# Performance work log

Hardware: AMD Instinct MI355X
Metric: run time of the kernel (lower is better)

The kernel has to match this reference:

```python
import jax, jax.numpy as jnp
import numpy as np

N = 100000   # nodes
E = 1600000  # edges (avg degree 16)
D = 128      # input/output dim
H = 128      # hidden dim
EPS = 1e-5


def _lin_init(key, fan_in, shape):
    s = 1.0 / np.sqrt(fan_in)
    return jax.random.uniform(key, shape, jnp.float32, minval=-s, maxval=s)


def setup_inputs() -> dict:
    key = jax.random.key(0)
    ks = jax.random.split(key, 12)
    x = jax.random.normal(ks[0], (N, D), jnp.float32)
    edge_index = jax.random.randint(ks[1], (2, E), 0, N, dtype=jnp.int64)
    return {
        "x": x,
        "edge_index": edge_index,
        # SAGEConv 1: lin_l (on aggregated, with bias), lin_r (root, no bias)
        "Wl1": _lin_init(ks[2], D, (D, H)),
        "bl1": jnp.zeros((H,), jnp.float32),
        "Wr1": _lin_init(ks[3], D, (D, H)),
        # graph LayerNorm 1 affine
        "g1": jnp.ones((H,), jnp.float32),
        "b1": jnp.zeros((H,), jnp.float32),
        # SAGEConv 2
        "Wl2": _lin_init(ks[4], H, (H, D)),
        "bl2": jnp.zeros((D,), jnp.float32),
        "Wr2": _lin_init(ks[5], H, (H, D)),
        # graph LayerNorm 2 affine
        "g2": jnp.ones((D,), jnp.float32),
        "b2": jnp.zeros((D,), jnp.float32),
    }


def graph_layernorm(h, gamma, beta):
    # PyG norm.LayerNorm mode='graph': normalize over ALL nodes and channels.
    mu = h.mean()
    hc = h - mu
    var = (hc * hc).mean()
    return hc * jax.lax.rsqrt(var + EPS) * gamma + beta


def sage_mean(h, src, dst, Wl, bl, Wr):
    # mean-aggregate source features at destination nodes
    msg = h[src]                                            # [E, C] gather
    ssum = jax.ops.segment_sum(msg, dst, num_segments=N)    # [N, C]
    cnt = jax.ops.segment_sum(jnp.ones((src.shape[0], 1), h.dtype), dst,
                              num_segments=N)               # [N, 1]
    agg = ssum / jnp.maximum(cnt, 1.0)
    return agg @ Wl + bl + h @ Wr


def reference(x, edge_index, Wl1, bl1, Wr1, g1, b1, Wl2, bl2, Wr2, g2, b2):
    src, dst = edge_index[0], edge_index[1]
    res = x
    h = jax.nn.relu(graph_layernorm(sage_mean(x, src, dst, Wl1, bl1, Wr1), g1, b1))
    h = jax.nn.relu(graph_layernorm(sage_mean(h, src, dst, Wl2, bl2, Wr2), g2, b2))
    return h + res
```

## Files before the change

### kernel.cpp

```cpp
#include <hip/hip_runtime.h>

typedef float  f32x4 __attribute__((ext_vector_type(4)));
typedef float  f32x2 __attribute__((ext_vector_type(2)));
typedef short  s16x8 __attribute__((ext_vector_type(8)));

#define BSHIFT 7
#define BMASK  127
#define CHUNK  8192

__device__ __forceinline__ unsigned short f2bf(float f) {
  unsigned int u = __float_as_uint(f);
  unsigned int r = (u + 0x7FFFu + ((u >> 16) & 1u)) >> 16;
  return (unsigned short)r;
}

__device__ __forceinline__ uint2 pk8_fp8(const float* y) {
  int p0 = __builtin_amdgcn_cvt_pk_fp8_f32(y[0], y[1], 0, false);
  p0     = __builtin_amdgcn_cvt_pk_fp8_f32(y[2], y[3], p0, true);
  int p1 = __builtin_amdgcn_cvt_pk_fp8_f32(y[4], y[5], 0, false);
  p1     = __builtin_amdgcn_cvt_pk_fp8_f32(y[6], y[7], p1, true);
  return make_uint2((unsigned)p0, (unsigned)p1);
}


__global__ void __launch_bounds__(256) k_prep(
    const float* __restrict__ x, unsigned short* __restrict__ xh,
    unsigned int* __restrict__ xf8, size_t total8, int cvtBlocks,
    const float* __restrict__ W0, const float* __restrict__ W1,
    const float* __restrict__ W2, const float* __restrict__ W3,
    unsigned short* __restrict__ B0, unsigned short* __restrict__ B1,
    unsigned short* __restrict__ B2, unsigned short* __restrict__ B3,
    const int* __restrict__ ei, int E, int* __restrict__ bhist, int NB) {
  __shared__ int h[1024];
  int b = blockIdx.x;
  if (b < cvtBlocks) {
    size_t i = (size_t)b * 256 + threadIdx.x;
    if (i >= total8) return;
    float4 a = ((const float4*)x)[i * 2];
    float4 c = ((const float4*)x)[i * 2 + 1];
    uint4 o;
    o.x = (unsigned)f2bf(a.x) | ((unsigned)f2bf(a.y) << 16);
    o.y = (unsigned)f2bf(a.z) | ((unsigned)f2bf(a.w) << 16);
    o.z = (unsigned)f2bf(c.x) | ((unsigned)f2bf(c.y) << 16);
    o.w = (unsigned)f2bf(c.z) | ((unsigned)f2bf(c.w) << 16);
    ((uint4*)xh)[i] = o;
    float y[8] = {a.x, a.y, a.z, a.w, c.x, c.y, c.z, c.w};
    ((uint2*)xf8)[i] = pk8_fp8(y);
  } else if (b < cvtBlocks + 32) {
    int gt = (b - cvtBlocks) * 256 + threadIdx.x;
    int which = gt >> 11;
    const float* W = which == 0 ? W0 : which == 1 ? W1 : which == 2 ? W2 : W3;
    unsigned short* WB = which == 0 ? B0 : which == 1 ? B1 : which == 2 ? B2 : B3;
    int t = gt & 2047;
    int lane = t & 63, kt = (t >> 6) & 3, nt = t >> 8;
    int col = nt * 16 + (lane & 15);
    int k0  = kt * 32 + ((lane >> 4) << 3);
#pragma unroll
    for (int j = 0; j < 8; ++j)
      WB[(((nt * 4 + kt) * 64 + lane) << 3) + j] = f2bf(W[(size_t)(k0 + j) * 128 + col]);
  } else {
    int bb = b - cvtBlocks - 32;
    for (int i = threadIdx.x; i < 1024; i += 256) h[i] = 0;
    __syncthreads();
    int i0 = bb * 256 + threadIdx.x;
    int stride = 128 * 256;
    for (int e = i0; e < E; e += stride)
      atomicAdd(&h[ei[E + e] >> BSHIFT], 1);
    __syncthreads();
    for (int i = threadIdx.x; i < NB; i += 256)
      if (h[i]) atomicAdd(&bhist[i], h[i]);
  }
}


__global__ void k_bscan(const int* __restrict__ bhist, int* __restrict__ boff,
                        int* __restrict__ bcur, int NB, int E) {
  __shared__ int tot[256];
  int t = threadIdx.x;
  int v[4]; int s = 0;
#pragma unroll
  for (int j = 0; j < 4; ++j) {
    int idx = t * 4 + j;
    v[j] = (idx < NB) ? bhist[idx] : 0;
    s += v[j];
  }
  tot[t] = s; __syncthreads();
  for (int off = 1; off < 256; off <<= 1) {
    int x = (t >= off) ? tot[t - off] : 0;
    __syncthreads();
    tot[t] += x;
    __syncthreads();
  }
  int excl = (t > 0) ? tot[t - 1] : 0;
#pragma unroll
  for (int j = 0; j < 4; ++j) {
    int idx = t * 4 + j;
    if (idx < NB) { boff[idx] = excl; bcur[idx] = excl; }
    excl += v[j];
  }
  if (t == 0) boff[NB] = E;
}

__global__ void __launch_bounds__(512) k_part(
    const int* __restrict__ ei, int E, int* __restrict__ bcur,
    unsigned int* __restrict__ tmp, int NB) {
  __shared__ int lh[1024], lbase[1024], lcur[1024];
  int t = threadIdx.x;
  int c0 = blockIdx.x * CHUNK;
  int cend = min(c0 + CHUNK, E);
  for (int i = t; i < NB; i += 512) lh[i] = 0;
  __syncthreads();
  for (int e = c0 + t; e < cend; e += 512)
    atomicAdd(&lh[ei[E + e] >> BSHIFT], 1);
  __syncthreads();
  for (int i = t; i < NB; i += 512) {
    int c = lh[i];
    lbase[i] = c ? atomicAdd(&bcur[i], c) : 0;
    lcur[i] = 0;
  }
  __syncthreads();
  for (int e = c0 + t; e < cend; e += 512) {
    int src = ei[e], dst = ei[E + e];
    int b = dst >> BSHIFT;
    int pos = lbase[b] + atomicAdd(&lcur[b], 1);
    tmp[pos] = ((unsigned)(dst & BMASK) << 25) | (unsigned)src;
  }
}

__global__ void __launch_bounds__(256) k_csr(
    const unsigned int* __restrict__ tmp, const int* __restrict__ boff,
    int* __restrict__ rowptr, int* __restrict__ ssrc, int N, int NB, int E) {
  __shared__ int cnt[128], sc[128], curs[128];
  int b = blockIdx.x;
  int t = threadIdx.x;
  int beg = boff[b], end = boff[b + 1];
  int nbase = b << BSHIFT;
  int nn = min(128, N - nbase);
  if (t < 128) cnt[t] = 0;
  __syncthreads();
  for (int i = beg + t; i < end; i += 256)
    atomicAdd(&cnt[tmp[i] >> 25], 1);
  __syncthreads();
  if (t < 128) sc[t] = cnt[t];
  __syncthreads();
  for (int off = 1; off < 128; off <<= 1) {
    int x = 0;
    if (t < 128 && t >= off) x = sc[t - off];
    __syncthreads();
    if (t < 128) sc[t] += x;
    __syncthreads();
  }
  if (t < nn) {
    int excl = sc[t] - cnt[t];
    rowptr[nbase + t] = beg + excl;
    curs[t] = excl;
  }
  __syncthreads();
  for (int i = beg + t; i < end; i += 256) {
    unsigned int p = tmp[i];
    int pos = beg + atomicAdd(&curs[p >> 25], 1);
    ssrc[pos] = (int)((p & 0x1FFFFFFu) << 7);
  }
  if (b == NB - 1 && t == 0) rowptr[N] = E;
}


__global__ void __launch_bounds__(256, 8) k_fmm(
    const unsigned char* __restrict__ featf8, const unsigned short* __restrict__ featbf,
    const int* __restrict__ rowptr, const int* __restrict__ ssrc,
    const unsigned short* __restrict__ WlB, const unsigned short* __restrict__ WrB,
    const float* __restrict__ bias, unsigned short* __restrict__ out,
    double* __restrict__ red, int N) {
  __shared__ __align__(16) unsigned short aggLds[64 * 136];
  int t = threadIdx.x;
  int l = t & 63, w = t >> 6;
  const char* fp = (const char*)featf8;

  {
    int gg = l >> 3;
    int sub = l & 7;
    unsigned suboff = (unsigned)(sub * 16);
#pragma unroll
    for (int j = 0; j < 2; ++j) {
      int row = w * 16 + gg * 2 + j;
      int node = blockIdx.x * 64 + row;
      if (node < N) {
        int beg = rowptr[node], end = rowptr[node + 1];
        f32x2 a0 = {0.f, 0.f}, a1 = a0, a2 = a0, a3 = a0,
              a4 = a0, a5 = a0, a6 = a0, a7 = a0;
#define ACCQ(q) {                                                        \
          a0 += __builtin_amdgcn_cvt_pk_f32_fp8((q).x, false);           \
          a1 += __builtin_amdgcn_cvt_pk_f32_fp8((q).x, true);            \
          a2 += __builtin_amdgcn_cvt_pk_f32_fp8((q).y, false);           \
          a3 += __builtin_amdgcn_cvt_pk_f32_fp8((q).y, true);            \
          a4 += __builtin_amdgcn_cvt_pk_f32_fp8((q).z, false);           \
          a5 += __builtin_amdgcn_cvt_pk_f32_fp8((q).z, true);            \
          a6 += __builtin_amdgcn_cvt_pk_f32_fp8((q).w, false);           \
          a7 += __builtin_amdgcn_cvt_pk_f32_fp8((q).w, true);            \
        }
        int i = beg;
        for (; i + 4 <= end; i += 4) {
          unsigned o0 = (unsigned)ssrc[i]     + suboff;
          unsigned o1 = (unsigned)ssrc[i + 1] + suboff;
          unsigned o2 = (unsigned)ssrc[i + 2] + suboff;
          unsigned o3 = (unsigned)ssrc[i + 3] + suboff;
          uint4 q0 = *(const uint4*)(fp + o0);
          uint4 q1 = *(const uint4*)(fp + o1);
          uint4 q2 = *(const uint4*)(fp + o2);
          uint4 q3 = *(const uint4*)(fp + o3);
          ACCQ(q0); ACCQ(q1); ACCQ(q2); ACCQ(q3);
        }
        for (; i < end; ++i) {
          uint4 q = *(const uint4*)(fp + ((unsigned)ssrc[i] + suboff));
          ACCQ(q);
        }
#undef ACCQ
        float inv = __builtin_amdgcn_rcpf(fmaxf((float)(end - beg), 1.0f));
        uint4 oa, ob;
        oa.x = (unsigned)f2bf(a0.x * inv) | ((unsigned)f2bf(a0.y * inv) << 16);
        oa.y = (unsigned)f2bf(a1.x * inv) | ((unsigned)f2bf(a1.y * inv) << 16);
        oa.z = (unsigned)f2bf(a2.x * inv) | ((unsigned)f2bf(a2.y * inv) << 16);
        oa.w = (unsigned)f2bf(a3.x * inv) | ((unsigned)f2bf(a3.y * inv) << 16);
        ob.x = (unsigned)f2bf(a4.x * inv) | ((unsigned)f2bf(a4.y * inv) << 16);
        ob.y = (unsigned)f2bf(a5.x * inv) | ((unsigned)f2bf(a5.y * inv) << 16);
        ob.z = (unsigned)f2bf(a6.x * inv) | ((unsigned)f2bf(a6.y * inv) << 16);
        ob.w = (unsigned)f2bf(a7.x * inv) | ((unsigned)f2bf(a7.y * inv) << 16);
        *(uint4*)&aggLds[row * 136 + sub * 16] = oa;
        *(uint4*)&aggLds[row * 136 + sub * 16 + 8] = ob;
      } else {
        uint4 z = make_uint4(0, 0, 0, 0);
        *(uint4*)&aggLds[row * 136 + sub * 16] = z;
        *(uint4*)&aggLds[row * 136 + sub * 16 + 8] = z;
      }
    }
  }

  int r0 = blockIdx.x * 64 + w * 16;
  int c = l & 15;
  int rb = (l >> 4) << 2;
  int rowA = r0 + c;
  int rowAc = min(rowA, N - 1);
  const size_t goff = (size_t)rowAc * 128 + ((l >> 4) << 3);
  const unsigned short* aLds = &aggLds[(w * 16 + c) * 136 + ((l >> 4) << 3)];

  f32x4 acc[8];
#pragma unroll
  for (int nt = 0; nt < 8; ++nt) acc[nt] = (f32x4){0.f, 0.f, 0.f, 0.f};

#pragma unroll
  for (int kt = 0; kt < 4; ++kt) {
    s16x8 a = *(const s16x8*)(aLds + kt * 32);
#pragma unroll
    for (int nt = 0; nt < 8; ++nt) {
      s16x8 b;
      { uint4 q = *(const uint4*)(WlB + (((nt * 4 + kt) * 64 + l) << 3));
        b = *(const s16x8*)&q; }
      acc[nt] = __builtin_amdgcn_mfma_f32_16x16x32_bf16(a, b, acc[nt], 0, 0, 0);
    }
  }
#pragma unroll
  for (int kt = 0; kt < 4; ++kt) {
    s16x8 a;
    { uint4 q = *(const uint4*)(featbf + goff + kt * 32);
      a = *(const s16x8*)&q; }
#pragma unroll
    for (int nt = 0; nt < 8; ++nt) {
      s16x8 b;
      { uint4 q = *(const uint4*)(WrB + (((nt * 4 + kt) * 64 + l) << 3));
        b = *(const s16x8*)&q; }
      acc[nt] = __builtin_amdgcn_mfma_f32_16x16x32_bf16(a, b, acc[nt], 0, 0, 0);
    }
  }

  float s = 0.f, s2 = 0.f;
#pragma unroll
  for (int nt = 0; nt < 8; ++nt) {
    float bv = bias[nt * 16 + c];
#pragma unroll
    for (int i = 0; i < 4; ++i) {
      float v = acc[nt][i] + bv;
      if (r0 + rb + i < N) { s += v; s2 += v * v; }
      aggLds[(w * 16 + rb + i) * 136 + nt * 16 + c] = f2bf(v);
    }
  }

#pragma unroll
  for (int j = 0; j < 4; ++j) {
    int idx = j * 64 + l;
    int riw = idx >> 4;
    int chunk = idx & 15;
    int row = r0 + riw;
    if (row < N) {
      uint4 o = *(const uint4*)&aggLds[(w * 16 + riw) * 136 + chunk * 8];
      *(uint4*)(out + (size_t)row * 128 + chunk * 8) = o;
    }
  }

#pragma unroll
  for (int off = 1; off < 64; off <<= 1) {
    s  += __shfl_xor(s, off);
    s2 += __shfl_xor(s2, off);
  }
  if (l == 0) {
    int bucket = (blockIdx.x * 4 + w) & 255;
    atomicAdd(&red[2 * bucket],     (double)s);
    atomicAdd(&red[2 * bucket + 1], (double)s2);
  }
}


__global__ void __launch_bounds__(256) k_apply1(
    const unsigned short* __restrict__ h, unsigned short* __restrict__ o,
    unsigned int* __restrict__ of8,
    const double* __restrict__ red, double count,
    const float* __restrict__ gamma, const float* __restrict__ beta,
    size_t total8) {
  __shared__ double sh[256], sh2[256];
  __shared__ float sc[2];
  int t = threadIdx.x;
  sh[t] = red[2 * t]; sh2[t] = red[2 * t + 1];
  __syncthreads();
  for (int off = 128; off > 0; off >>= 1) {
    if (t < off) { sh[t] += sh[t + off]; sh2[t] += sh2[t + off]; }
    __syncthreads();
  }
  if (t == 0) {
    double mu = sh[0] / count;
    double var = sh2[0] / count - mu * mu;
    sc[0] = (float)mu;
    sc[1] = (float)(1.0 / sqrt(var + 1e-5));
  }
  __syncthreads();
  size_t i = (size_t)blockIdx.x * blockDim.x + t;
  if (i >= total8) return;
  float mu = sc[0], rs = sc[1];
  int c0 = (int)((i * 8) & 127);
  float4 g0 = *(const float4*)(gamma + c0);
  float4 g1 = *(const float4*)(gamma + c0 + 4);
  float4 b0 = *(const float4*)(beta + c0);
  float4 b1 = *(const float4*)(beta + c0 + 4);
  uint4 q = ((const uint4*)h)[i];
  float gg[8] = {g0.x, g0.y, g0.z, g0.w, g1.x, g1.y, g1.z, g1.w};
  float bb[8] = {b0.x, b0.y, b0.z, b0.w, b1.x, b1.y, b1.z, b1.w};
  uint4 ov;
  float y[8];
#pragma unroll
  for (int w = 0; w < 4; ++w) {
    unsigned int v = ((const unsigned int*)&q)[w];
    float x0 = __uint_as_float(v << 16);
    float x1 = __uint_as_float(v & 0xFFFF0000u);
    float y0 = fmaxf((x0 - mu) * rs * gg[2 * w] + bb[2 * w], 0.f);
    float y1 = fmaxf((x1 - mu) * rs * gg[2 * w + 1] + bb[2 * w + 1], 0.f);
    y[2 * w] = y0; y[2 * w + 1] = y1;
    ((unsigned int*)&ov)[w] = (unsigned)f2bf(y0) | ((unsigned)f2bf(y1) << 16);
  }
  ((uint4*)o)[i] = ov;
  ((uint2*)of8)[i] = pk8_fp8(y);
}


__global__ void __launch_bounds__(256) k_apply2(
    const unsigned short* __restrict__ h, const unsigned short* __restrict__ xres,
    float* __restrict__ o, const double* __restrict__ red, double count,
    const float* __restrict__ gamma, const float* __restrict__ beta,
    size_t total8) {
  __shared__ double sh[256], sh2[256];
  __shared__ float sc[2];
  int t = threadIdx.x;
  sh[t] = red[2 * t]; sh2[t] = red[2 * t + 1];
  __syncthreads();
  for (int off = 128; off > 0; off >>= 1) {
    if (t < off) { sh[t] += sh[t + off]; sh2[t] += sh2[t + off]; }
    __syncthreads();
  }
  if (t == 0) {
    double mu = sh[0] / count;
    double var = sh2[0] / count - mu * mu;
    sc[0] = (float)mu;
    sc[1] = (float)(1.0 / sqrt(var + 1e-5));
  }
  __syncthreads();
  size_t i = (size_t)blockIdx.x * blockDim.x + t;
  if (i >= total8) return;
  float mu = sc[0], rs = sc[1];
  int c0 = (int)((i * 8) & 127);
  float4 g0 = *(const float4*)(gamma + c0);
  float4 g1 = *(const float4*)(gamma + c0 + 4);
  float4 b0 = *(const float4*)(beta + c0);
  float4 b1 = *(const float4*)(beta + c0 + 4);
  uint4 q  = ((const uint4*)h)[i];
  uint4 qx = ((const uint4*)xres)[i];
  float gg[8] = {g0.x, g0.y, g0.z, g0.w, g1.x, g1.y, g1.z, g1.w};
  float bb[8] = {b0.x, b0.y, b0.z, b0.w, b1.x, b1.y, b1.z, b1.w};
  float out8[8];
#pragma unroll
  for (int w = 0; w < 4; ++w) {
    unsigned int v  = ((const unsigned int*)&q)[w];
    unsigned int vx = ((const unsigned int*)&qx)[w];
    float x0 = __uint_as_float(v << 16);
    float x1 = __uint_as_float(v & 0xFFFF0000u);
    float r0 = __uint_as_float(vx << 16);
    float r1 = __uint_as_float(vx & 0xFFFF0000u);
    out8[2 * w]     = fmaxf((x0 - mu) * rs * gg[2 * w] + bb[2 * w], 0.f) + r0;
    out8[2 * w + 1] = fmaxf((x1 - mu) * rs * gg[2 * w + 1] + bb[2 * w + 1], 0.f) + r1;
  }
  ((float4*)o)[i * 2]     = make_float4(out8[0], out8[1], out8[2], out8[3]);
  ((float4*)o)[i * 2 + 1] = make_float4(out8[4], out8[5], out8[6], out8[7]);
}


extern "C" void kernel_launch(void* const* d_in, const int* in_sizes, int n_in,
                              void* d_out, int out_size, void* d_ws, size_t ws_size,
                              hipStream_t stream) {
  const float* x   = (const float*)d_in[0];
  const int*   ei  = (const int*)d_in[1];
  const float* Wl1 = (const float*)d_in[2];
  const float* bl1 = (const float*)d_in[3];
  const float* Wr1 = (const float*)d_in[4];
  const float* g1  = (const float*)d_in[5];
  const float* b1  = (const float*)d_in[6];
  const float* Wl2 = (const float*)d_in[7];
  const float* bl2 = (const float*)d_in[8];
  const float* Wr2 = (const float*)d_in[9];
  const float* g2  = (const float*)d_in[10];
  const float* b2  = (const float*)d_in[11];
  float* out = (float*)d_out;

  const int N = in_sizes[0] / 128;
  const int E = in_sizes[1] / 2;
  const int NB = (N + BMASK) >> BSHIFT;

  char* ws = (char*)d_ws;
  size_t off = 0;
  auto alloc = [&](size_t bytes) -> void* {
    void* p = ws + off;
    off = (off + bytes + 255) & ~(size_t)255;
    return p;
  };
  unsigned short* xh   = (unsigned short*)alloc((size_t)N * 128 * 2);
  unsigned short* hmm  = (unsigned short*)alloc((size_t)N * 128 * 2);
  unsigned short* h1n  = (unsigned short*)alloc((size_t)N * 128 * 2);
  unsigned int*   xf8  = (unsigned int*)alloc((size_t)N * 128);
  unsigned int*   h1f8 = (unsigned int*)alloc((size_t)N * 128);
  int*    ssrc   = (int*)alloc((size_t)E * 4);
  int*    rowptr = (int*)alloc((size_t)(N + 1) * 4);
  int*    bhist  = (int*)alloc((size_t)(NB + 1) * 4);
  double* red    = (double*)alloc(2 * 512 * sizeof(double));
  int*    boff   = (int*)alloc((size_t)(NB + 1) * 4);
  int*    bcur   = (int*)alloc((size_t)(NB + 1) * 4);
  unsigned short* Wl1b = (unsigned short*)alloc(128 * 128 * 2);
  unsigned short* Wr1b = (unsigned short*)alloc(128 * 128 * 2);
  unsigned short* Wl2b = (unsigned short*)alloc(128 * 128 * 2);
  unsigned short* Wr2b = (unsigned short*)alloc(128 * 128 * 2);
  unsigned int* tmp = (unsigned int*)hmm;
  (void)ws_size; (void)n_in; (void)out_size;

  const size_t total  = (size_t)N * 128;
  const size_t total8 = total / 8;
  const int applyGrid = (int)((total8 + 255) / 256);

  hipMemsetAsync(bhist, 0, (size_t)((char*)(red + 2 * 512) - (char*)bhist), stream);

  k_prep<<<applyGrid + 32 + 128, 256, 0, stream>>>(
      x, xh, xf8, total8, applyGrid,
      Wl1, Wr1, Wl2, Wr2, Wl1b, Wr1b, Wl2b, Wr2b,
      ei, E, bhist, NB);
  k_bscan<<<1, 256, 0, stream>>>(bhist, boff, bcur, NB, E);
  k_part<<<(E + CHUNK - 1) / CHUNK, 512, 0, stream>>>(ei, E, bcur, tmp, NB);
  k_csr<<<NB, 256, 0, stream>>>(tmp, boff, rowptr, ssrc, N, NB, E);

  const int mmGrid = (N + 63) / 64;

  k_fmm<<<mmGrid, 256, 0, stream>>>((const unsigned char*)xf8, xh, rowptr, ssrc,
                                    Wl1b, Wr1b, bl1, hmm, red, N);
  k_apply1<<<applyGrid, 256, 0, stream>>>(hmm, h1n, h1f8, red, (double)total, g1, b1, total8);

  k_fmm<<<mmGrid, 256, 0, stream>>>((const unsigned char*)h1f8, h1n, rowptr, ssrc,
                                    Wl2b, Wr2b, bl2, hmm, red + 512, N);
  k_apply2<<<applyGrid, 256, 0, stream>>>(hmm, xh, out, red + 512, (double)total, g2, b2, total8);
}
```

Measured before the change: 221.7 us.

## Fuse graph LayerNorm apply into SAGE matmul via cooperative grid sync

Turns the matmul kernel into a cooperative kernel that keeps its bf16 output tile in LDS, does a grid-wide sync after the mean/variance atomics, then applies LayerNorm, ReLU, and the residual or fp8 repack directly from LDS. This removes the hmm write and re-read and the two separate apply launches. In exchange it needs the whole grid (1563 blocks) resident, which depends on reaching 8 blocks per CU; otherwise it falls back to the old path. Every launch now also pays host attribute and occupancy queries, and all blocks stall at the grid barrier.

```diff
diff --git a/kernel.cpp b/kernel.cpp
--- a/kernel.cpp
+++ b/kernel.cpp
@@ -1,4 +1,7 @@
 #include <hip/hip_runtime.h>
+#include <hip/hip_cooperative_groups.h>
+
+namespace cg = cooperative_groups;
 
 typedef float  f32x4 __attribute__((ext_vector_type(4)));
 typedef float  f32x2 __attribute__((ext_vector_type(2)));
@@ -165,13 +168,18 @@
 }
 
 
-__global__ void __launch_bounds__(256, 8) k_fmm(
+__global__ void __launch_bounds__(256, 8) k_fmm_ln(
     const unsigned char* __restrict__ featf8, const unsigned short* __restrict__ featbf,
     const int* __restrict__ rowptr, const int* __restrict__ ssrc,
     const unsigned short* __restrict__ WlB, const unsigned short* __restrict__ WrB,
-    const float* __restrict__ bias, unsigned short* __restrict__ out,
-    double* __restrict__ red, int N) {
+    const float* __restrict__ bias, const float* __restrict__ gamma,
+    const float* __restrict__ beta, double* __restrict__ red,
+    int N, double count, int mode,
+    unsigned short* __restrict__ o_bf, unsigned int* __restrict__ o_f8,
+    const unsigned short* __restrict__ xres, float* __restrict__ o_f32) {
   __shared__ __align__(16) unsigned short aggLds[64 * 136];
+  __shared__ double shd[4][2];
+  __shared__ float scb[2];
   int t = threadIdx.x;
   int l = t & 63, w = t >> 6;
   const char* fp = (const char*)featf8;
@@ -283,7 +291,211 @@
       aggLds[(w * 16 + rb + i) * 136 + nt * 16 + c] = f2bf(v);
     }
   }
-
+#pragma unroll
+  for (int off = 1; off < 64; off <<= 1) {
+    s  += __shfl_xor(s, off);
+    s2 += __shfl_xor(s2, off);
+  }
+  if (l == 0) {
+    int bucket = (blockIdx.x * 4 + w) & 255;
+    atomicAdd(&red[2 * bucket],     (double)s);
+    atomicAdd(&red[2 * bucket + 1], (double)s2);
+  }
+
+  cg::this_grid().sync();
+
+  {
+    double a = red[2 * t], b = red[2 * t + 1];
+#pragma unroll
+    for (int off = 1; off < 64; off <<= 1) {
+      a += __shfl_xor(a, off);
+      b += __shfl_xor(b, off);
+    }
+    if (l == 0) { shd[w][0] = a; shd[w][1] = b; }
+    __syncthreads();
+    if (t == 0) {
+      double su = shd[0][0] + shd[1][0] + shd[2][0] + shd[3][0];
+      double sq = shd[0][1] + shd[1][1] + shd[2][1] + shd[3][1];
+      double mu = su / count;
+      double var = sq / count - mu * mu;
+      scb[0] = (float)mu;
+      scb[1] = (float)(1.0 / sqrt(var + 1e-5));
+    }
+    __syncthreads();
+  }
+  float mu = scb[0], rs = scb[1];
+
+#pragma unroll
+  for (int j = 0; j < 4; ++j) {
+    int idx = j * 64 + l;
+    int riw = idx >> 4;
+    int chunk = idx & 15;
+    int row = r0 + riw;
+    if (row < N) {
+      uint4 q = *(const uint4*)&aggLds[(w * 16 + riw) * 136 + chunk * 8];
+      int c0 = chunk * 8;
+      float4 g0 = *(const float4*)(gamma + c0);
+      float4 g1 = *(const float4*)(gamma + c0 + 4);
+      float4 b0 = *(const float4*)(beta + c0);
+      float4 b1 = *(const float4*)(beta + c0 + 4);
+      float gg[8] = {g0.x, g0.y, g0.z, g0.w, g1.x, g1.y, g1.z, g1.w};
+      float bb[8] = {b0.x, b0.y, b0.z, b0.w, b1.x, b1.y, b1.z, b1.w};
+      float y[8];
+#pragma unroll
+      for (int k = 0; k < 4; ++k) {
+        unsigned int v = ((const unsigned int*)&q)[k];
+        float x0 = __uint_as_float(v << 16);
+        float x1 = __uint_as_float(v & 0xFFFF0000u);
+        y[2 * k]     = fmaxf((x0 - mu) * rs * gg[2 * k] + bb[2 * k], 0.f);
+        y[2 * k + 1] = fmaxf((x1 - mu) * rs * gg[2 * k + 1] + bb[2 * k + 1], 0.f);
+      }
+      if (mode == 0) {
+        uint4 ov;
+#pragma unroll
+        for (int k = 0; k < 4; ++k)
+          ((unsigned int*)&ov)[k] = (unsigned)f2bf(y[2 * k]) |
+                                    ((unsigned)f2bf(y[2 * k + 1]) << 16);
+        *(uint4*)(o_bf + (size_t)row * 128 + c0) = ov;
+        ((uint2*)o_f8)[(size_t)row * 16 + chunk] = pk8_fp8(y);
+      } else {
+        uint4 qx = *(const uint4*)(xres + (size_t)row * 128 + c0);
+        float4 oA, oB;
+        {
+          unsigned int vx = qx.x;
+          oA.x = y[0] + __uint_as_float(vx << 16);
+          oA.y = y[1] + __uint_as_float(vx & 0xFFFF0000u);
+          vx = qx.y;
+          oA.z = y[2] + __uint_as_float(vx << 16);
+          oA.w = y[3] + __uint_as_float(vx & 0xFFFF0000u);
+          vx = qx.z;
+          oB.x = y[4] + __uint_as_float(vx << 16);
+          oB.y = y[5] + __uint_as_float(vx & 0xFFFF0000u);
+          vx = qx.w;
+          oB.z = y[6] + __uint_as_float(vx << 16);
+          oB.w = y[7] + __uint_as_float(vx & 0xFFFF0000u);
+        }
+        float* op = o_f32 + (size_t)row * 128 + c0;
+        *(float4*)op = oA;
+        *(float4*)(op + 4) = oB;
+      }
+    }
+  }
+}
+
+
+__global__ void __launch_bounds__(256, 8) k_fmm(
+    const unsigned char* __restrict__ featf8, const unsigned short* __restrict__ featbf,
+    const int* __restrict__ rowptr, const int* __restrict__ ssrc,
+    const unsigned short* __restrict__ WlB, const unsigned short* __restrict__ WrB,
+    const float* __restrict__ bias, unsigned short* __restrict__ out,
+    double* __restrict__ red, int N) {
+  __shared__ __align__(16) unsigned short aggLds[64 * 136];
+  int t = threadIdx.x;
+  int l = t & 63, w = t >> 6;
+  const char* fp = (const char*)featf8;
+  {
+    int gg = l >> 3;
+    int sub = l & 7;
+    unsigned suboff = (unsigned)(sub * 16);
+#pragma unroll
+    for (int j = 0; j < 2; ++j) {
+      int row = w * 16 + gg * 2 + j;
+      int node = blockIdx.x * 64 + row;
+      if (node < N) {
+        int beg = rowptr[node], end = rowptr[node + 1];
+        f32x2 a0 = {0.f, 0.f}, a1 = a0, a2 = a0, a3 = a0,
+              a4 = a0, a5 = a0, a6 = a0, a7 = a0;
+#define ACCQ(q) {                                                        \
+          a0 += __builtin_amdgcn_cvt_pk_f32_fp8((q).x, false);           \
+          a1 += __builtin_amdgcn_cvt_pk_f32_fp8((q).x, true);            \
+          a2 += __builtin_amdgcn_cvt_pk_f32_fp8((q).y, false);           \
+          a3 += __builtin_amdgcn_cvt_pk_f32_fp8((q).y, true);            \
+          a4 += __builtin_amdgcn_cvt_pk_f32_fp8((q).z, false);           \
+          a5 += __builtin_amdgcn_cvt_pk_f32_fp8((q).z, true);            \
+          a6 += __builtin_amdgcn_cvt_pk_f32_fp8((q).w, false);           \
+          a7 += __builtin_amdgcn_cvt_pk_f32_fp8((q).w, true);            \
+        }
+        int i = beg;
+        for (; i + 4 <= end; i += 4) {
+          unsigned o0 = (unsigned)ssrc[i]     + suboff;
+          unsigned o1 = (unsigned)ssrc[i + 1] + suboff;
+          unsigned o2 = (unsigned)ssrc[i + 2] + suboff;
+          unsigned o3 = (unsigned)ssrc[i + 3] + suboff;
+          uint4 q0 = *(const uint4*)(fp + o0);
+          uint4 q1 = *(const uint4*)(fp + o1);
+          uint4 q2 = *(const uint4*)(fp + o2);
+          uint4 q3 = *(const uint4*)(fp + o3);
+          ACCQ(q0); ACCQ(q1); ACCQ(q2); ACCQ(q3);
+        }
+        for (; i < end; ++i) {
+          uint4 q = *(const uint4*)(fp + ((unsigned)ssrc[i] + suboff));
+          ACCQ(q);
+        }
+#undef ACCQ
+        float inv = __builtin_amdgcn_rcpf(fmaxf((float)(end - beg), 1.0f));
+        uint4 oa, ob;
+        oa.x = (unsigned)f2bf(a0.x * inv) | ((unsigned)f2bf(a0.y * inv) << 16);
+        oa.y = (unsigned)f2bf(a1.x * inv) | ((unsigned)f2bf(a1.y * inv) << 16);
+        oa.z = (unsigned)f2bf(a2.x * inv) | ((unsigned)f2bf(a2.y * inv) << 16);
+        oa.w = (unsigned)f2bf(a3.x * inv) | ((unsigned)f2bf(a3.y * inv) << 16);
+        ob.x = (unsigned)f2bf(a4.x * inv) | ((unsigned)f2bf(a4.y * inv) << 16);
+        ob.y = (unsigned)f2bf(a5.x * inv) | ((unsigned)f2bf(a5.y * inv) << 16);
+        ob.z = (unsigned)f2bf(a6.x * inv) | ((unsigned)f2bf(a6.y * inv) << 16);
+        ob.w = (unsigned)f2bf(a7.x * inv) | ((unsigned)f2bf(a7.y * inv) << 16);
+        *(uint4*)&aggLds[row * 136 + sub * 16] = oa;
+        *(uint4*)&aggLds[row * 136 + sub * 16 + 8] = ob;
+      } else {
+        uint4 z = make_uint4(0, 0, 0, 0);
+        *(uint4*)&aggLds[row * 136 + sub * 16] = z;
+        *(uint4*)&aggLds[row * 136 + sub * 16 + 8] = z;
+      }
+    }
+  }
+  int r0 = blockIdx.x * 64 + w * 16;
+  int c = l & 15;
+  int rb = (l >> 4) << 2;
+  int rowA = r0 + c;
+  int rowAc = min(rowA, N - 1);
+  const size_t goff = (size_t)rowAc * 128 + ((l >> 4) << 3);
+  const unsigned short* aLds = &aggLds[(w * 16 + c) * 136 + ((l >> 4) << 3)];
+  f32x4 acc[8];
+#pragma unroll
+  for (int nt = 0; nt < 8; ++nt) acc[nt] = (f32x4){0.f, 0.f, 0.f, 0.f};
+#pragma unroll
+  for (int kt = 0; kt < 4; ++kt) {
+    s16x8 a = *(const s16x8*)(aLds + kt * 32);
+#pragma unroll
+    for (int nt = 0; nt < 8; ++nt) {
+      s16x8 b;
+      { uint4 q = *(const uint4*)(WlB + (((nt * 4 + kt) * 64 + l) << 3));
+        b = *(const s16x8*)&q; }
+      acc[nt] = __builtin_amdgcn_mfma_f32_16x16x32_bf16(a, b, acc[nt], 0, 0, 0);
+    }
+  }
+#pragma unroll
+  for (int kt = 0; kt < 4; ++kt) {
+    s16x8 a;
+    { uint4 q = *(const uint4*)(featbf + goff + kt * 32);
+      a = *(const s16x8*)&q; }
+#pragma unroll
+    for (int nt = 0; nt < 8; ++nt) {
+      s16x8 b;
+      { uint4 q = *(const uint4*)(WrB + (((nt * 4 + kt) * 64 + l) << 3));
+        b = *(const s16x8*)&q; }
+      acc[nt] = __builtin_amdgcn_mfma_f32_16x16x32_bf16(a, b, acc[nt], 0, 0, 0);
+    }
+  }
+  float s = 0.f, s2 = 0.f;
+#pragma unroll
+  for (int nt = 0; nt < 8; ++nt) {
+    float bv = bias[nt * 16 + c];
+#pragma unroll
+    for (int i = 0; i < 4; ++i) {
+      float v = acc[nt][i] + bv;
+      if (r0 + rb + i < N) { s += v; s2 += v * v; }
+      aggLds[(w * 16 + rb + i) * 136 + nt * 16 + c] = f2bf(v);
+    }
+  }
 #pragma unroll
   for (int j = 0; j < 4; ++j) {
     int idx = j * 64 + l;
@@ -295,7 +507,6 @@
       *(uint4*)(out + (size_t)row * 128 + chunk * 8) = o;
     }
   }
-
 #pragma unroll
   for (int off = 1; off < 64; off <<= 1) {
     s  += __shfl_xor(s, off);
@@ -307,7 +518,6 @@
     atomicAdd(&red[2 * bucket + 1], (double)s2);
   }
 }
-
 
 __global__ void __launch_bounds__(256) k_apply1(
     const unsigned short* __restrict__ h, unsigned short* __restrict__ o,
@@ -357,7 +567,6 @@
   ((uint4*)o)[i] = ov;
   ((uint2*)of8)[i] = pk8_fp8(y);
 }
-
 
 __global__ void __launch_bounds__(256) k_apply2(
     const unsigned short* __restrict__ h, const unsigned short* __restrict__ xres,
@@ -471,11 +680,42 @@
 
   const int mmGrid = (N + 63) / 64;
 
-  k_fmm<<<mmGrid, 256, 0, stream>>>((const unsigned char*)xf8, xh, rowptr, ssrc,
-                                    Wl1b, Wr1b, bl1, hmm, red, N);
-  k_apply1<<<applyGrid, 256, 0, stream>>>(hmm, h1n, h1f8, red, (double)total, g1, b1, total8);
-
-  k_fmm<<<mmGrid, 256, 0, stream>>>((const unsigned char*)h1f8, h1n, rowptr, ssrc,
-                                    Wl2b, Wr2b, bl2, hmm, red + 512, N);
-  k_apply2<<<applyGrid, 256, 0, stream>>>(hmm, xh, out, red + 512, (double)total, g2, b2, total8);
-}
+  int coop = 0;
+  hipDeviceGetAttribute(&coop, hipDeviceAttributeCooperativeLaunch, 0);
+  int maxBlocksPerCU = 0;
+  hipOccupancyMaxActiveBlocksPerMultiprocessor(&maxBlocksPerCU, (const void*)k_fmm_ln, 256, 0);
+  hipDeviceProp_t prop;
+  hipGetDeviceProperties(&prop, 0);
+  bool fused = coop && ((long)maxBlocksPerCU * prop.multiProcessorCount >= mmGrid);
+
+  if (fused) {
+    const unsigned char* xf8c  = (const unsigned char*)xf8;
+    const unsigned char* h1f8c = (const unsigned char*)h1f8;
+    int Nv = N; double cnt = (double)total;
+    int m0 = 0, m1 = 1;
+    double* red1 = red; double* red2 = red + 512;
+    const unsigned short* xhc = xh;
+    const unsigned short* h1nc = h1n;
+    unsigned short* nb = nullptr; unsigned int* nf8 = nullptr;
+    const unsigned short* nx = nullptr; float* nf = nullptr;
+
+    void* a1[] = {(void*)&xf8c, (void*)&xhc, (void*)&rowptr, (void*)&ssrc,
+                  (void*)&Wl1b, (void*)&Wr1b, (void*)&bl1, (void*)&g1, (void*)&b1,
+                  (void*)&red1, (void*)&Nv, (void*)&cnt, (void*)&m0,
+                  (void*)&h1n, (void*)&h1f8, (void*)&nx, (void*)&nf};
+    hipLaunchCooperativeKernel((void*)k_fmm_ln, dim3(mmGrid), dim3(256), a1, 0, stream);
+
+    void* a2[] = {(void*)&h1f8c, (void*)&h1nc, (void*)&rowptr, (void*)&ssrc,
+                  (void*)&Wl2b, (void*)&Wr2b, (void*)&bl2, (void*)&g2, (void*)&b2,
+                  (void*)&red2, (void*)&Nv, (void*)&cnt, (void*)&m1,
+                  (void*)&nb, (void*)&nf8, (void*)&xhc, (void*)&out};
+    hipLaunchCooperativeKernel((void*)k_fmm_ln, dim3(mmGrid), dim3(256), a2, 0, stream);
+  } else {
+    k_fmm<<<mmGrid, 256, 0, stream>>>((const unsigned char*)xf8, xh, rowptr, ssrc,
+                                      Wl1b, Wr1b, bl1, hmm, red, N);
+    k_apply1<<<applyGrid, 256, 0, stream>>>(hmm, h1n, h1f8, red, (double)total, g1, b1, total8);
+    k_fmm<<<mmGrid, 256, 0, stream>>>((const unsigned char*)h1f8, h1n, rowptr, ssrc,
+                                      Wl2b, Wr2b, bl2, hmm, red + 512, N);
+    k_apply2<<<applyGrid, 256, 0, stream>>>(hmm, xh, out, red + 512, (double)total, g2, b2, total8);
+  }
+}
```

Result: no change. 218.1 us, median of 2 (-1.6%).
